# Performance work log

Hardware: AMD Instinct MI355X
Metric: run time of the kernel (lower is better)

Reference implementation:

```python
import jax, jax.numpy as jnp
import numpy as np

NUM_HEADS = 16
ROPE_THETA = 1000.0


def _rope(x, cos, sin):
    # x: [B, H, T, d_k]; cos/sin: [T, d_k//2]
    xp = x.reshape(x.shape[:-1] + (x.shape[-1] // 2, 2))
    xe, xo = xp[..., 0], xp[..., 1]
    c = cos[None, None, :, :]
    s = sin[None, None, :, :]
    re = xe * c - xo * s
    ro = xe * s + xo * c
    return jnp.stack((re, ro), axis=-1).reshape(x.shape)


def setup_inputs() -> dict:
    key = jax.random.key(0)
    ks = jax.random.split(key, 5)
    B, T, D = 2, 2048, 1024
    std = 2.0 / (D + D)
    return {
        "x": jax.random.normal(ks[0], (B, T, D), dtype=jnp.float32),
        "wq": jax.random.normal(ks[1], (D, D), dtype=jnp.float32) * std,
        "wk": jax.random.normal(ks[2], (D, D), dtype=jnp.float32) * std,
        "wv": jax.random.normal(ks[3], (D, D), dtype=jnp.float32) * std,
        "wo": jax.random.normal(ks[4], (D, D), dtype=jnp.float32) * std,
    }


def reference(x, wq, wk, wv, wo):
    B, T, D = x.shape
    H = NUM_HEADS
    dk = D // H

    def proj(w):
        # Linear stores weight as [out, in]: '... in, out in -> ... out'
        y = jnp.einsum('btd,ed->bte', x, w)
        return y.reshape(B, T, H, dk).transpose(0, 2, 1, 3)  # [B,H,T,dk]

    q = proj(wq)
    k = proj(wk)
    v = proj(wv)

    # RoPE tables
    pos = jnp.arange(T, dtype=jnp.float32)[:, None]
    kidx = jnp.arange(dk // 2, dtype=jnp.float32)
    inv_freq = ROPE_THETA ** (-2.0 * kidx / dk)
    ang = pos * inv_freq[None, :]
    cos, sin = jnp.cos(ang), jnp.sin(ang)

    q = _rope(q, cos, sin)
    k = _rope(k, cos, sin)

    scores = jnp.einsum('bhnd,bhmd->bhnm', q, k) / jnp.sqrt(jnp.asarray(dk, x.dtype))
    causal = jnp.tril(jnp.ones((T, T), dtype=bool))
    scores = jnp.where(causal[None, None], scores, -jnp.inf)
    attn = jax.nn.softmax(scores, axis=-1)
    head = jnp.einsum('bhnm,bhmd->bhnd', attn, v)  # [B,H,T,dk]

    concat = head.transpose(0, 2, 1, 3).reshape(B, T, D)
    return jnp.einsum('btd,ed->bte', concat, wo)
```

## Files before the change

kernel.cpp:

```cpp
#include <hip/hip_runtime.h>
#include <hip/hip_bf16.h>

typedef __hip_bfloat16 bf16;
typedef __attribute__((ext_vector_type(8))) short bf16x8;
typedef __attribute__((ext_vector_type(4))) float f32x4;

#define T_SEQ 2048
#define NHEADS 16
#define DK 64
#define DMODEL 1024

__device__ inline void load_lds16(const void* g, void* l) {
    __builtin_amdgcn_global_load_lds((const __attribute__((address_space(1))) void*)g,
                                     (__attribute__((address_space(3))) void*)l, 16, 0, 0);
}

__global__ void cvt_all(const float* __restrict__ x,  const float* __restrict__ wq,
                        const float* __restrict__ wk, const float* __restrict__ wv,
                        const float* __restrict__ wo, bf16* __restrict__ xb,
                        bf16* __restrict__ wqkvb, bf16* __restrict__ wob) {
    int i = blockIdx.x * blockDim.x + threadIdx.x;
    const float* src; bf16* dst; int off;
    if (i < (1 << 20)) { src = x; dst = xb; off = i; }
    else {
        int j = i - (1 << 20);
        int seg = j >> 18; off = j & ((1 << 18) - 1);
        src = (seg == 0) ? wq : (seg == 1) ? wk : (seg == 2) ? wv : wo;
        dst = (seg < 3) ? (wqkvb + ((size_t)seg << 20)) : wob;
    }
    float4 f = ((const float4*)src)[off];
    ushort4 o;
    o.x = __bfloat16_as_ushort(__float2bfloat16(f.x));
    o.y = __bfloat16_as_ushort(__float2bfloat16(f.y));
    o.z = __bfloat16_as_ushort(__float2bfloat16(f.z));
    o.w = __bfloat16_as_ushort(__float2bfloat16(f.w));
    ((ushort4*)dst)[off] = o;
}

__global__ __launch_bounds__(256) void gemm_qkv_rope(const bf16* __restrict__ A,
                                                     const bf16* __restrict__ B,
                                                     bf16* __restrict__ qb,
                                                     bf16* __restrict__ kb,
                                                     bf16* __restrict__ vt) {
    const int K = 1024, N = 3072;
    __shared__ bf16 As[128 * 32];
    __shared__ bf16 Bs[128 * 32];
    const int tid  = threadIdx.x;
    const int lane = tid & 63;
    const int wave = tid >> 6;
    const int l16  = lane & 15;
    const int quad = lane >> 4;
    const int wy = wave >> 1, wx = wave & 1;
    const int brow = blockIdx.y * 128;
    const int bcol = blockIdx.x * 128;

    f32x4 acc[4][4] = {};

    for (int k0 = 0; k0 < K; k0 += 32) {
#pragma unroll
        for (int i = 0; i < 2; ++i) {
            int j   = tid + 256 * i;
            int row = j >> 2;
            int cc  = j & 3;
            load_lds16(A + (size_t)(brow + row) * K + k0 + cc * 8, (char*)As + j * 16);
            load_lds16(B + (size_t)(bcol + row) * K + k0 + cc * 8, (char*)Bs + j * 16);
        }
        __syncthreads();
        bf16x8 af[4], bq[4];
#pragma unroll
        for (int i = 0; i < 4; ++i)
            af[i] = *(const bf16x8*)(As + (wy * 64 + i * 16 + l16) * 32 + quad * 8);
#pragma unroll
        for (int j = 0; j < 4; ++j)
            bq[j] = *(const bf16x8*)(Bs + (wx * 64 + j * 16 + l16) * 32 + quad * 8);
#pragma unroll
        for (int i = 0; i < 4; ++i)
#pragma unroll
            for (int j = 0; j < 4; ++j)
                acc[i][j] = __builtin_amdgcn_mfma_f32_16x16x32_bf16(af[i], bq[j], acc[i][j], 0, 0, 0);
        __syncthreads();
    }
    const int seg = bcol >> 10;
    const int hh  = ((bcol & 1023) >> 6) + wx;
    if (seg < 2) {
        bf16* dst = seg ? kb : qb;
        const float osc = seg ? 1.0f : 0.18033688011112042f;
#pragma unroll
        for (int j = 0; j < 4; ++j) {
            const int d = j * 16 + l16;
            const float inv = exp2f(-0.31143075889f * (float)(d >> 1));
#pragma unroll
            for (int i = 0; i < 4; ++i)
#pragma unroll
                for (int r = 0; r < 4; ++r) {
                    int row = brow + wy * 64 + i * 16 + quad * 4 + r;
                    int t = row & (T_SEQ - 1), bi = row >> 11;
                    float s, c;
                    __sincosf((float)t * inv, &s, &c);
                    float v = acc[i][j][r];
                    float p = __shfl_xor(v, 1);
                    float res = (l16 & 1) ? fmaf(p, s, v * c) : fmaf(-p, s, v * c);
                    dst[((size_t)(bi * NHEADS + hh) * T_SEQ + t) * DK + d] =
                        __float2bfloat16(res * osc);
                }
        }
    } else {
#pragma unroll
        for (int j = 0; j < 4; ++j) {
            const int d = j * 16 + l16;
#pragma unroll
            for (int i = 0; i < 4; ++i)
#pragma unroll
                for (int r = 0; r < 4; ++r) {
                    int row = brow + wy * 64 + i * 16 + quad * 4 + r;
                    int t = row & (T_SEQ - 1), bi = row >> 11;
                    vt[((size_t)(bi * NHEADS + hh) * DK + d) * T_SEQ + t] =
                        __float2bfloat16(acc[i][j][r]);
                }
        }
    }
}

__global__ __launch_bounds__(256) void gemm_bt(const bf16* __restrict__ A,
                                               const bf16* __restrict__ B,
                                               float* __restrict__ C,
                                               int M, int N, int K) {
    __shared__ bf16 As[128 * 32];
    __shared__ bf16 Bs[128 * 32];
    const int tid  = threadIdx.x;
    const int lane = tid & 63;
    const int wave = tid >> 6;
    const int l16  = lane & 15;
    const int quad = lane >> 4;
    const int wy = wave >> 1, wx = wave & 1;
    const int brow = blockIdx.y * 128;
    const int bcol = blockIdx.x * 128;

    f32x4 acc[4][4] = {};

    for (int k0 = 0; k0 < K; k0 += 32) {
#pragma unroll
        for (int i = 0; i < 2; ++i) {
            int j   = tid + 256 * i;
            int row = j >> 2;
            int cc  = j & 3;
            load_lds16(A + (size_t)(brow + row) * K + k0 + cc * 8, (char*)As + j * 16);
            load_lds16(B + (size_t)(bcol + row) * K + k0 + cc * 8, (char*)Bs + j * 16);
        }
        __syncthreads();
        bf16x8 af[4], bq[4];
#pragma unroll
        for (int i = 0; i < 4; ++i)
            af[i] = *(const bf16x8*)(As + (wy * 64 + i * 16 + l16) * 32 + quad * 8);
#pragma unroll
        for (int j = 0; j < 4; ++j)
            bq[j] = *(const bf16x8*)(Bs + (wx * 64 + j * 16 + l16) * 32 + quad * 8);
#pragma unroll
        for (int i = 0; i < 4; ++i)
#pragma unroll
            for (int j = 0; j < 4; ++j)
                acc[i][j] = __builtin_amdgcn_mfma_f32_16x16x32_bf16(af[i], bq[j], acc[i][j], 0, 0, 0);
        __syncthreads();
    }
#pragma unroll
    for (int i = 0; i < 4; ++i)
#pragma unroll
        for (int j = 0; j < 4; ++j)
#pragma unroll
            for (int r = 0; r < 4; ++r) {
                int row = brow + wy * 64 + i * 16 + quad * 4 + r;
                int col = bcol + wx * 64 + j * 16 + l16;
                C[(size_t)row * N + col] = acc[i][j][r];
            }
}

__constant__ unsigned char c_sched[24] = {
    28, 61, 57, 58, 24, 53, 49, 20,
    62, 54, 50, 41, 42, 16, 45, 46,
     0,  4,  8, 12, 33, 37, 34, 38};

__global__ __launch_bounds__(256, 4) void attn_kernel(const bf16* __restrict__ qb,
                                                      const bf16* __restrict__ kb,
                                                      const bf16* __restrict__ vt,
                                                      float* __restrict__ Oacc,
                                                      float* __restrict__ Lacc,
                                                      bf16* __restrict__ conc) {
    __shared__ bf16 Ks[2][64 * 64];
    __shared__ bf16 Vs[2][64 * 64];
    __shared__ bf16 Pl[4][16 * 64];
    const int bh = blockIdx.y;
    const int b = bh >> 4, h = bh & 15;

    const int e    = c_sched[blockIdx.x];
    const int tile = e >> 2, mode = e & 3;
    const int it0  = (mode == 2) ? tile + 1 : 0;
    const int it1  = (mode == 1) ? tile : 2 * tile + 1;
    const bool partial = (mode != 0);
    const int qbase = tile << 7;

    const int tid = threadIdx.x;
    const int lane = tid & 63, wave = tid >> 6;
    const int l16 = lane & 15, quad = lane >> 4;
    const int qr0 = qbase + wave * 16;
    const int qr1 = qr0 + 64;

    const bf16* Qp = qb + (size_t)bh * T_SEQ * DK;
    const bf16* Kp = kb + (size_t)bh * T_SEQ * DK;
    const bf16* Vp = vt + (size_t)bh * DK * T_SEQ;
    char* Pw = (char*)&Pl[wave][0];

    const short one_bits = 0x3F80;
    const bf16x8 ones = {one_bits, one_bits, one_bits, one_bits,
                         one_bits, one_bits, one_bits, one_bits};

    bf16x8 qf[2][2];
#pragma unroll
    for (int s = 0; s < 2; ++s) {
        qf[0][s] = *(const bf16x8*)(Qp + (size_t)(qr0 + l16) * DK + s * 32 + quad * 8);
        qf[1][s] = *(const bf16x8*)(Qp + (size_t)(qr1 + l16) * DK + s * 32 + quad * 8);
    }

    auto stage = [&](int bb, int k0) {
        int j = tid;
#pragma unroll
        for (int i = 0; i < 2; ++i, j += 256) {
            int row = j >> 3, cbl = (j & 7) ^ ((j >> 3) & 7);
            load_lds16(Kp + (size_t)(k0 + row) * DK + cbl * 8, (char*)Ks[bb] + j * 16);
        }
        j = tid;
#pragma unroll
        for (int i = 0; i < 2; ++i, j += 256) {
            int row = j >> 3, cbl = (j & 7) ^ ((j >> 3) & 7);
            load_lds16(Vp + (size_t)row * T_SEQ + k0 + cbl * 8, (char*)Vs[bb] + j * 16);
        }
    };

    f32x4 o0[4] = {}, o1[4] = {};
    f32x4 ol0 = {}, ol1 = {};
    const int sw0 = (quad ^ (l16 & 7)) * 8;
    const int sw1 = ((4 + quad) ^ (l16 & 7)) * 8;
    const int pw_wr_base = l16 * 128 + (quad & 1) * 8;
    const int pq = quad >> 1, pql = quad & 1;

    int cur = 0;
    stage(0, it0 * 64);
    for (int it = it0; it <= it1; ++it) {
        __syncthreads();
        if (it < it1) stage(cur ^ 1, (it + 1) * 64);

        const int k0 = it * 64;
        const bool skip0 = (k0 > qr0 + 15);
        const bool diag0 = (k0 + 63 > qr0) && !skip0;
        const bool diag1 = (k0 + 63 > qr1);

        f32x4 s0[4] = {}, s1[4] = {};
        __builtin_amdgcn_s_setprio(1);
#pragma unroll
        for (int nt = 0; nt < 4; ++nt) {
            bf16x8 kf0 = *(const bf16x8*)(Ks[cur] + (nt * 16 + l16) * 64 + sw0);
            bf16x8 kf1 = *(const bf16x8*)(Ks[cur] + (nt * 16 + l16) * 64 + sw1);
            if (!skip0) {
                s0[nt] = __builtin_amdgcn_mfma_f32_16x16x32_bf16(kf0, qf[0][0], s0[nt], 0, 0, 0);
                s0[nt] = __builtin_amdgcn_mfma_f32_16x16x32_bf16(kf1, qf[0][1], s0[nt], 0, 0, 0);
            }
            s1[nt] = __builtin_amdgcn_mfma_f32_16x16x32_bf16(kf0, qf[1][0], s1[nt], 0, 0, 0);
            s1[nt] = __builtin_amdgcn_mfma_f32_16x16x32_bf16(kf1, qf[1][1], s1[nt], 0, 0, 0);
        }
        __builtin_amdgcn_s_setprio(0);

        if (!skip0) {
#pragma unroll
            for (int nt = 0; nt < 4; ++nt) {
                union { bf16 hv[4]; uint2 u; } pk;
#pragma unroll
                for (int r = 0; r < 4; ++r) {
                    float v = s0[nt][r];
                    if (diag0 && (k0 + nt * 16 + quad * 4 + r > qr0 + l16)) v = -30.0f;
                    pk.hv[r] = __float2bfloat16(exp2f(v));
                }
                *(uint2*)(Pw + pw_wr_base + (((nt * 2 + pq) ^ (l16 & 7)) << 4)) = pk.u;
            }
            __builtin_amdgcn_s_setprio(1);
#pragma unroll
            for (int ks = 0; ks < 2; ++ks) {
                bf16x8 pf = *(const bf16x8*)(Pw + l16 * 128 + (((ks * 4 + quad) ^ (l16 & 7)) << 4));
                const int sw = ks ? sw1 : sw0;
                ol0 = __builtin_amdgcn_mfma_f32_16x16x32_bf16(pf, ones, ol0, 0, 0, 0);
#pragma unroll
                for (int j = 0; j < 4; ++j) {
                    bf16x8 vf = *(const bf16x8*)(Vs[cur] + (j * 16 + l16) * 64 + sw);
                    o0[j] = __builtin_amdgcn_mfma_f32_16x16x32_bf16(pf, vf, o0[j], 0, 0, 0);
                }
            }
            __builtin_amdgcn_s_setprio(0);
        }

#pragma unroll
        for (int nt = 0; nt < 4; ++nt) {
            union { bf16 hv[4]; uint2 u; } pk;
#pragma unroll
            for (int r = 0; r < 4; ++r) {
                float v = s1[nt][r];
                if (diag1 && (k0 + nt * 16 + quad * 4 + r > qr1 + l16)) v = -30.0f;
                pk.hv[r] = __float2bfloat16(exp2f(v));
            }
            *(uint2*)(Pw + pw_wr_base + (((nt * 2 + pq) ^ (l16 & 7)) << 4)) = pk.u;
        }
        __builtin_amdgcn_s_setprio(1);
#pragma unroll
        for (int ks = 0; ks < 2; ++ks) {
            bf16x8 pf = *(const bf16x8*)(Pw + l16 * 128 + (((ks * 4 + quad) ^ (l16 & 7)) << 4));
            const int sw = ks ? sw1 : sw0;
            ol1 = __builtin_amdgcn_mfma_f32_16x16x32_bf16(pf, ones, ol1, 0, 0, 0);
#pragma unroll
            for (int j = 0; j < 4; ++j) {
                bf16x8 vf = *(const bf16x8*)(Vs[cur] + (j * 16 + l16) * 64 + sw);
                o1[j] = __builtin_amdgcn_mfma_f32_16x16x32_bf16(pf, vf, o1[j], 0, 0, 0);
            }
        }
        __builtin_amdgcn_s_setprio(0);
        cur ^= 1;
    }

#pragma unroll
    for (int g = 0; g < 2; ++g) {
        const f32x4* op = g ? o1 : o0;
        const f32x4 lv = g ? ol1 : ol0;
        const int qr = g ? qr1 : qr0;
        if (!partial) {
#pragma unroll
            for (int r = 0; r < 4; ++r) {
                float inv_l = 1.0f / lv[r];
                int t = qr + quad * 4 + r;
#pragma unroll
                for (int j = 0; j < 4; ++j)
                    conc[((size_t)b * T_SEQ + t) * DMODEL + h * DK + j * 16 + l16] =
                        __float2bfloat16(op[j][r] * inv_l);
            }
        } else {
#pragma unroll
            for (int r = 0; r < 4; ++r) {
                int q = qr + quad * 4 + r;
                if (l16 == 0)
                    atomicAdd(&Lacc[(size_t)bh * 1024 + q - 1024], lv[r]);
                float* Ob = Oacc + ((size_t)bh * 1024 + q - 1024) * DK;
#pragma unroll
                for (int j = 0; j < 4; ++j)
                    atomicAdd(&Ob[j * 16 + l16], op[j][r]);
            }
        }
    }
}

__global__ void attn_finalize(const float* __restrict__ Oacc, const float* __restrict__ Lacc,
                              bf16* __restrict__ conc) {
    int i4 = blockIdx.x * blockDim.x + threadIdx.x;
    if (i4 >= (1 << 19)) return;
    int bhq = i4 >> 4;
    int d4  = i4 & 15;
    int bh = bhq >> 10, q1 = bhq & 1023;
    int b = bh >> 4, h = bh & 15;
    int q = 1024 + q1;
    float inv = 1.0f / Lacc[bhq];
    float4 o4 = ((const float4*)Oacc)[i4];
    ushort4 u;
    u.x = __bfloat16_as_ushort(__float2bfloat16(o4.x * inv));
    u.y = __bfloat16_as_ushort(__float2bfloat16(o4.y * inv));
    u.z = __bfloat16_as_ushort(__float2bfloat16(o4.z * inv));
    u.w = __bfloat16_as_ushort(__float2bfloat16(o4.w * inv));
    *(ushort4*)&conc[((size_t)(b * T_SEQ + q)) * DMODEL + h * DK + d4 * 4] = u;
}

extern "C" void kernel_launch(void* const* d_in, const int* in_sizes, int n_in,
                              void* d_out, int out_size, void* d_ws, size_t ws_size,
                              hipStream_t stream) {
    const float* x  = (const float*)d_in[0];
    const float* wq = (const float*)d_in[1];
    const float* wk = (const float*)d_in[2];
    const float* wv = (const float*)d_in[3];
    const float* wo = (const float*)d_in[4];
    float* out = (float*)d_out;

    char* ws = (char*)d_ws;
    bf16* xb    = (bf16*)(ws);
    bf16* wqkvb = (bf16*)(ws + (8ull << 20));
    bf16* wob   = (bf16*)(ws + (14ull << 20));
    bf16* qb    = (bf16*)(ws + (40ull << 20));
    bf16* kb    = (bf16*)(ws + (48ull << 20));
    bf16* vt    = (bf16*)(ws + (56ull << 20));
    bf16* conc  = (bf16*)(ws + (16ull << 20));
    float* Oacc = (float*)(ws + (24ull << 20));
    float* Lacc = (float*)(ws + (32ull << 20));

    cvt_all<<<8192, 256, 0, stream>>>(x, wq, wk, wv, wo, xb, wqkvb, wob);
    gemm_qkv_rope<<<dim3(24, 32), 256, 0, stream>>>(xb, wqkvb, qb, kb, vt);

    hipMemsetAsync(Oacc, 0, (8ull << 20) + 32 * 1024 * sizeof(float), stream);
    attn_kernel<<<dim3(24, 32), 256, 0, stream>>>(qb, kb, vt, Oacc, Lacc, conc);
    attn_finalize<<<2048, 256, 0, stream>>>(Oacc, Lacc, conc);

    gemm_bt<<<dim3(8, 32), 256, 0, stream>>>(conc, wob, out, 4096, 1024, 1024);
}
```

Before: 209.9 us.

## Swizzle GEMM LDS tiles, precompute RoPE table, transpose V-tile MFMA for coalesced stores

Applies an XOR swizzle to the LDS A/B tile layout in both GEMM kernels to reduce bank conflicts on the 16-byte fragment reads. Replaces the per-element sincos in the QKV epilogue with lookups into a precomputed cos/sin table built by a new small kernel. For the V segment it swaps the MFMA operands, so the accumulator comes out transposed and the transposed V stores run contiguously along t. This adds an extra kernel launch and table reads from memory in exchange for less epilogue math and better store coalescing.

```diff
diff --git a/kernel.cpp b/kernel.cpp
--- a/kernel.cpp
+++ b/kernel.cpp
@@ -13,6 +13,15 @@
 __device__ inline void load_lds16(const void* g, void* l) {
     __builtin_amdgcn_global_load_lds((const __attribute__((address_space(1))) void*)g,
                                      (__attribute__((address_space(3))) void*)l, 16, 0, 0);
+}
+
+__global__ void rope_table_k(float2* __restrict__ tab) {
+    int idx = blockIdx.x * blockDim.x + threadIdx.x;
+    int t = idx >> 5, i = idx & 31;
+    float inv = exp2f(-0.31143075889f * (float)i);
+    float s, c;
+    __sincosf((float)t * inv, &s, &c);
+    tab[idx] = make_float2(c, s);
 }
 
 __global__ void cvt_all(const float* __restrict__ x,  const float* __restrict__ wq,
@@ -39,10 +48,11 @@
 
 __global__ __launch_bounds__(256) void gemm_qkv_rope(const bf16* __restrict__ A,
                                                      const bf16* __restrict__ B,
+                                                     const float2* __restrict__ tab,
                                                      bf16* __restrict__ qb,
                                                      bf16* __restrict__ kb,
                                                      bf16* __restrict__ vt) {
-    const int K = 1024, N = 3072;
+    const int K = 1024;
     __shared__ bf16 As[128 * 32];
     __shared__ bf16 Bs[128 * 32];
     const int tid  = threadIdx.x;
@@ -53,6 +63,7 @@
     const int wy = wave >> 1, wx = wave & 1;
     const int brow = blockIdx.y * 128;
     const int bcol = blockIdx.x * 128;
+    const int seg  = bcol >> 10;
 
     f32x4 acc[4][4] = {};
 
@@ -61,63 +72,72 @@
         for (int i = 0; i < 2; ++i) {
             int j   = tid + 256 * i;
             int row = j >> 2;
-            int cc  = j & 3;
+            int cc  = (j & 3) ^ ((row >> 1) & 3);
             load_lds16(A + (size_t)(brow + row) * K + k0 + cc * 8, (char*)As + j * 16);
             load_lds16(B + (size_t)(bcol + row) * K + k0 + cc * 8, (char*)Bs + j * 16);
         }
         __syncthreads();
         bf16x8 af[4], bq[4];
 #pragma unroll
-        for (int i = 0; i < 4; ++i)
-            af[i] = *(const bf16x8*)(As + (wy * 64 + i * 16 + l16) * 32 + quad * 8);
-#pragma unroll
-        for (int j = 0; j < 4; ++j)
-            bq[j] = *(const bf16x8*)(Bs + (wx * 64 + j * 16 + l16) * 32 + quad * 8);
-#pragma unroll
-        for (int i = 0; i < 4; ++i)
-#pragma unroll
-            for (int j = 0; j < 4; ++j)
-                acc[i][j] = __builtin_amdgcn_mfma_f32_16x16x32_bf16(af[i], bq[j], acc[i][j], 0, 0, 0);
+        for (int i = 0; i < 4; ++i) {
+            int row = wy * 64 + i * 16 + l16;
+            af[i] = *(const bf16x8*)(As + row * 32 + (quad ^ ((row >> 1) & 3)) * 8);
+        }
+#pragma unroll
+        for (int j = 0; j < 4; ++j) {
+            int row = wx * 64 + j * 16 + l16;
+            bq[j] = *(const bf16x8*)(Bs + row * 32 + (quad ^ ((row >> 1) & 3)) * 8);
+        }
+        if (seg < 2) {
+#pragma unroll
+            for (int i = 0; i < 4; ++i)
+#pragma unroll
+                for (int j = 0; j < 4; ++j)
+                    acc[i][j] = __builtin_amdgcn_mfma_f32_16x16x32_bf16(af[i], bq[j], acc[i][j], 0, 0, 0);
+        } else {
+#pragma unroll
+            for (int i = 0; i < 4; ++i)
+#pragma unroll
+                for (int j = 0; j < 4; ++j)
+                    acc[i][j] = __builtin_amdgcn_mfma_f32_16x16x32_bf16(bq[j], af[i], acc[i][j], 0, 0, 0);
+        }
         __syncthreads();
     }
-    const int seg = bcol >> 10;
-    const int hh  = ((bcol & 1023) >> 6) + wx;
+    const int hh = ((bcol & 1023) >> 6) + wx;
     if (seg < 2) {
         bf16* dst = seg ? kb : qb;
         const float osc = seg ? 1.0f : 0.18033688011112042f;
 #pragma unroll
         for (int j = 0; j < 4; ++j) {
-            const int d = j * 16 + l16;
-            const float inv = exp2f(-0.31143075889f * (float)(d >> 1));
+            const int fidx = j * 8 + (l16 >> 1);
 #pragma unroll
             for (int i = 0; i < 4; ++i)
 #pragma unroll
                 for (int r = 0; r < 4; ++r) {
                     int row = brow + wy * 64 + i * 16 + quad * 4 + r;
                     int t = row & (T_SEQ - 1), bi = row >> 11;
-                    float s, c;
-                    __sincosf((float)t * inv, &s, &c);
+                    float2 cs = tab[t * 32 + fidx];
                     float v = acc[i][j][r];
                     float p = __shfl_xor(v, 1);
-                    float res = (l16 & 1) ? fmaf(p, s, v * c) : fmaf(-p, s, v * c);
-                    dst[((size_t)(bi * NHEADS + hh) * T_SEQ + t) * DK + d] =
+                    float res = (l16 & 1) ? fmaf(p, cs.y, v * cs.x)
+                                          : fmaf(-p, cs.y, v * cs.x);
+                    dst[((size_t)(bi * NHEADS + hh) * T_SEQ + t) * DK + j * 16 + l16] =
                         __float2bfloat16(res * osc);
                 }
         }
     } else {
 #pragma unroll
-        for (int j = 0; j < 4; ++j) {
-            const int d = j * 16 + l16;
+        for (int j = 0; j < 4; ++j)
 #pragma unroll
             for (int i = 0; i < 4; ++i)
 #pragma unroll
                 for (int r = 0; r < 4; ++r) {
-                    int row = brow + wy * 64 + i * 16 + quad * 4 + r;
-                    int t = row & (T_SEQ - 1), bi = row >> 11;
+                    int d    = j * 16 + quad * 4 + r;
+                    int tcol = brow + wy * 64 + i * 16 + l16;
+                    int t = tcol & (T_SEQ - 1), bi = tcol >> 11;
                     vt[((size_t)(bi * NHEADS + hh) * DK + d) * T_SEQ + t] =
                         __float2bfloat16(acc[i][j][r]);
                 }
-        }
     }
 }
 
@@ -143,18 +163,22 @@
         for (int i = 0; i < 2; ++i) {
             int j   = tid + 256 * i;
             int row = j >> 2;
-            int cc  = j & 3;
+            int cc  = (j & 3) ^ ((row >> 1) & 3);
             load_lds16(A + (size_t)(brow + row) * K + k0 + cc * 8, (char*)As + j * 16);
             load_lds16(B + (size_t)(bcol + row) * K + k0 + cc * 8, (char*)Bs + j * 16);
         }
         __syncthreads();
         bf16x8 af[4], bq[4];
 #pragma unroll
-        for (int i = 0; i < 4; ++i)
-            af[i] = *(const bf16x8*)(As + (wy * 64 + i * 16 + l16) * 32 + quad * 8);
-#pragma unroll
-        for (int j = 0; j < 4; ++j)
-            bq[j] = *(const bf16x8*)(Bs + (wx * 64 + j * 16 + l16) * 32 + quad * 8);
+        for (int i = 0; i < 4; ++i) {
+            int row = wy * 64 + i * 16 + l16;
+            af[i] = *(const bf16x8*)(As + row * 32 + (quad ^ ((row >> 1) & 3)) * 8);
+        }
+#pragma unroll
+        for (int j = 0; j < 4; ++j) {
+            int row = wx * 64 + j * 16 + l16;
+            bq[j] = *(const bf16x8*)(Bs + row * 32 + (quad ^ ((row >> 1) & 3)) * 8);
+        }
 #pragma unroll
         for (int i = 0; i < 4; ++i)
 #pragma unroll
@@ -240,7 +264,7 @@
     const int sw0 = (quad ^ (l16 & 7)) * 8;
     const int sw1 = ((4 + quad) ^ (l16 & 7)) * 8;
     const int pw_wr_base = l16 * 128 + (quad & 1) * 8;
-    const int pq = quad >> 1, pql = quad & 1;
+    const int pq = quad >> 1;
 
     int cur = 0;
     stage(0, it0 * 64);
@@ -391,9 +415,11 @@
     bf16* conc  = (bf16*)(ws + (16ull << 20));
     float* Oacc = (float*)(ws + (24ull << 20));
     float* Lacc = (float*)(ws + (32ull << 20));
-
+    float2* rtab = (float2*)(ws + (34ull << 20));
+
+    rope_table_k<<<256, 256, 0, stream>>>(rtab);
     cvt_all<<<8192, 256, 0, stream>>>(x, wq, wk, wv, wo, xb, wqkvb, wob);
-    gemm_qkv_rope<<<dim3(24, 32), 256, 0, stream>>>(xb, wqkvb, qb, kb, vt);
+    gemm_qkv_rope<<<dim3(24, 32), 256, 0, stream>>>(xb, wqkvb, rtab, qb, kb, vt);
 
     hipMemsetAsync(Oacc, 0, (8ull << 20) + 32 * 1024 * sizeof(float), stream);
     attn_kernel<<<dim3(24, 32), 256, 0, stream>>>(qb, kb, vt, Oacc, Lacc, conc);
```

Measured after the change: 243.1 us. 15.8% more time.
